# Performance work log

Hardware: AMD Instinct MI355X
Metric: run time of the kernel (lower is better)

The kernel has to match this reference:

```python
import jax, jax.numpy as jnp
import numpy as np

N_HEAD, D_MODEL, D_HEAD = 16, 1024, 64
BSZ, QLEN, KLEN = 4, 1024, 2048
MEM_LEN = KLEN - QLEN


def _rel_shift(x):
    # x: [b, q, k, n] -> Transformer-XL relative shift
    b, q, k, n = x.shape
    zero_pad = jnp.zeros((b, q, 1, n), dtype=x.dtype)
    x_padded = jnp.concatenate([zero_pad, x], axis=2)        # [b, q, k+1, n]
    x_padded = x_padded.reshape(b, k + 1, q, n)
    return x_padded[:, 1:].reshape(b, q, k, n)


def setup_inputs() -> dict:
    key = jax.random.key(0)
    ks = jax.random.split(key, 8)
    s = 0.02
    w = jax.random.normal(ks[0], (BSZ, KLEN, D_MODEL), jnp.float32)
    r = jax.random.normal(ks[1], (1, KLEN, D_MODEL), jnp.float32)
    r_w_bias = jax.random.normal(ks[2], (N_HEAD, D_HEAD), jnp.float32) * s
    r_r_bias = jax.random.normal(ks[3], (N_HEAD, D_HEAD), jnp.float32) * s
    Wq = jax.random.normal(ks[4], (D_MODEL, N_HEAD * D_HEAD), jnp.float32) * s
    Wkv = jax.random.normal(ks[5], (D_MODEL, 2 * N_HEAD * D_HEAD), jnp.float32) * s
    Wr = jax.random.normal(ks[6], (D_MODEL, N_HEAD * D_HEAD), jnp.float32) * s
    Wo = jax.random.normal(ks[7], (N_HEAD * D_HEAD, D_MODEL), jnp.float32) * s
    # causal mask with memory: query i attends to j <= i + MEM_LEN
    attn_mask = jnp.triu(jnp.ones((QLEN, KLEN), dtype=bool), k=MEM_LEN + 1)
    return {"w": w, "r": r, "r_w_bias": r_w_bias, "r_r_bias": r_r_bias,
            "Wq": Wq, "Wkv": Wkv, "Wr": Wr, "Wo": Wo,
            "attn_mask": attn_mask, "qlen": QLEN}


def reference(w, r, r_w_bias, r_r_bias, Wq, Wkv, Wr, Wo, attn_mask, qlen):
    bsz, klen, _ = w.shape
    rlen = r.shape[1]
    scale = 1.0 / (D_HEAD ** 0.5)

    q = (w[:, -qlen:] @ Wq).reshape(bsz, qlen, N_HEAD, D_HEAD)
    kv = w @ Wkv
    k, v = jnp.split(kv, 2, axis=-1)
    k = k.reshape(bsz, klen, N_HEAD, D_HEAD)
    v = v.reshape(bsz, klen, N_HEAD, D_HEAD)
    rk = (r[0] @ Wr).reshape(rlen, N_HEAD, D_HEAD)

    AC = jnp.einsum('bind,bjnd->bijn', q + r_w_bias, k)
    BD = jnp.einsum('bind,jnd->bijn', q + r_r_bias, rk)
    attn_score = (AC + _rel_shift(BD)) * scale
    attn_score = jnp.where(attn_mask[None, :, :, None], jnp.float32(-1e30), attn_score)
    attn_prob = jax.nn.softmax(attn_score, axis=2)
    attn_vec = jnp.einsum('bijn,bjnd->bind', attn_prob, v)
    attn_vec = attn_vec.reshape(bsz, qlen, N_HEAD * D_HEAD)
    return attn_vec @ Wo
```

## Files before the change

### kernel.cpp

```cpp
#include <hip/hip_runtime.h>

constexpr int BSZ  = 4;
constexpr int NH   = 16;
constexpr int DH   = 64;
constexpr int QL   = 1024;
constexpr int KLN  = 2048;
constexpr int DM   = 1024;
constexpr int MEM  = 1024;

typedef __bf16 bf16x8  __attribute__((ext_vector_type(8)));
typedef __bf16 bf16x4t __attribute__((ext_vector_type(4)));
typedef float  f32x4   __attribute__((ext_vector_type(4)));

__device__ __forceinline__ void g2l16(__bf16* lds, const __bf16* g) {
    __builtin_amdgcn_global_load_lds(
        (const __attribute__((address_space(1))) unsigned int*)g,
        (__attribute__((address_space(3))) unsigned int*)lds, 16, 0, 0);
}

__global__ __launch_bounds__(256)
void prep(const float* __restrict__ w, const float* __restrict__ r,
          const float* __restrict__ Wq, const float* __restrict__ Wr,
          const float* __restrict__ Wo, const float* __restrict__ Wkv,
          __bf16* __restrict__ wbh, __bf16* __restrict__ rbh,
          __bf16* __restrict__ WqT, __bf16* __restrict__ WrT,
          __bf16* __restrict__ WoT, __bf16* __restrict__ WkvT)
{
    __shared__ __bf16 t[64 * 72];
    const int id = blockIdx.x;
    if (id < 5120) {
        const float* in; __bf16* out; size_t i;
        if (id < 4096) { in = w; out = wbh; i = ((size_t)id * 256 + threadIdx.x) * 8; }
        else { in = r; out = rbh; i = ((size_t)(id - 4096) * 256 + threadIdx.x) * 8; }
        float4 a = *(const float4*)(in + i);
        float4 b = *(const float4*)(in + i + 4);
        bf16x8 y = {(__bf16)a.x, (__bf16)a.y, (__bf16)a.z, (__bf16)a.w,
                    (__bf16)b.x, (__bf16)b.y, (__bf16)b.z, (__bf16)b.w};
        *(bf16x8*)(out + i) = y;
        return;
    }
    const int tt = id - 5120;
    const int z = tt >> 9, rem = tt & 511;
    const int xx = rem & 31, yy = rem >> 5;
    const float* in; __bf16* out; int N;
    if (z == 0)      { in = Wq;  out = WqT;  N = 1024; }
    else if (z == 1) { in = Wr;  out = WrT;  N = 1024; }
    else if (z == 2) { in = Wo;  out = WoT;  N = 1024; }
    else             { in = Wkv; out = WkvT; N = 2048; }
    if (xx * 64 >= N) return;
    const int n0 = xx * 64, k0 = yy * 64;
    const int row = threadIdx.x >> 2, seg = (threadIdx.x & 3) << 4;
    const float* src = in + (long)(k0 + row) * N + n0 + seg;
#pragma unroll
    for (int u = 0; u < 16; u += 4) {
        float4 x = *(const float4*)(src + u);
        t[(seg + u + 0) * 72 + row] = (__bf16)x.x;
        t[(seg + u + 1) * 72 + row] = (__bf16)x.y;
        t[(seg + u + 2) * 72 + row] = (__bf16)x.z;
        t[(seg + u + 3) * 72 + row] = (__bf16)x.w;
    }
    __syncthreads();
    __bf16* dst = out + (long)(n0 + row) * 1024 + k0 + seg;
    *(uint4*)(dst)     = *(const uint4*)(t + row * 72 + seg);
    *(uint4*)(dst + 8) = *(const uint4*)(t + row * 72 + seg + 8);
}

__device__ __forceinline__ void gemm_core(
    const __bf16* __restrict__ A, const __bf16* __restrict__ BT,
    __bf16* As, __bf16* Bs, int m0, int n0, int K, f32x4 (&acc)[4][4])
{
    const int tid = threadIdx.x, w = tid >> 6, l = tid & 63;
    const int il = l & 15, quad = l >> 4;
    const int wm = (w >> 1) * 64, wn = (w & 1) * 64;
    const int lr = l >> 2, kc = (l & 3) ^ (lr & 3);

    const __bf16* ag = A  + (long)(m0 + w * 32 + lr) * K + kc * 8;
    const __bf16* bg = BT + (long)(n0 + w * 32 + lr) * K + kc * 8;
    __bf16* al0 = As + (w * 32) * 32;
    __bf16* al1 = As + (w * 32 + 16) * 32;
    __bf16* bl0 = Bs + (w * 32) * 32;
    __bf16* bl1 = Bs + (w * 32 + 16) * 32;
    const int rsw = il & 3;

    for (int k0 = 0; k0 < K; k0 += 32) {
        __syncthreads();
        g2l16(al0, ag + k0);
        g2l16(al1, ag + k0 + 16 * K);
        g2l16(bl0, bg + k0);
        g2l16(bl1, bg + k0 + 16 * K);
        __syncthreads();

        bf16x8 af[4], bf[4];
#pragma unroll
        for (int f = 0; f < 4; ++f) {
            af[f] = *(const bf16x8*)(As + (wm + f * 16 + il) * 32 + ((quad ^ rsw) << 3));
            bf[f] = *(const bf16x8*)(Bs + (wn + f * 16 + il) * 32 + ((quad ^ rsw) << 3));
        }
#pragma unroll
        for (int i = 0; i < 4; ++i)
#pragma unroll
            for (int j = 0; j < 4; ++j)
                acc[i][j] = __builtin_amdgcn_mfma_f32_16x16x32_bf16(
                    af[i], bf[j], acc[i][j], 0, 0, 0);
    }
}

__global__ __launch_bounds__(256, 2)
void gemm_proj(const __bf16* __restrict__ wbh, const __bf16* __restrict__ rbh,
               const __bf16* __restrict__ WqT, const __bf16* __restrict__ WkvT,
               const __bf16* __restrict__ WrT,
               __bf16* __restrict__ qwh, __bf16* __restrict__ qrh,
               __bf16* __restrict__ kh, __bf16* __restrict__ vhT,
               __bf16* __restrict__ rkh,
               const float* __restrict__ bw, const float* __restrict__ br)
{
    __shared__ __bf16 As[128 * 32];
    __shared__ __bf16 Bs[128 * 32];
    const int id = blockIdx.x;
    const __bf16 *A, *BT;
    int m0, n0, zz, kind;
    if (id < 1024) {
        n0 = (id & 15) * 128; m0 = ((id >> 4) & 15) * 128; zz = id >> 8;
        A = wbh + (size_t)zz * KLN * DM; BT = WkvT; kind = 3;
    } else if (id < 1280) {
        const int t = id - 1024;
        n0 = (t & 7) * 128; m0 = ((t >> 3) & 7) * 128; zz = t >> 6;
        A = wbh + (size_t)zz * KLN * DM + (size_t)MEM * DM; BT = WqT; kind = 2;
    } else {
        const int t = id - 1280;
        n0 = (t & 7) * 128; m0 = (t >> 3) * 128; zz = 0;
        A = rbh; BT = WrT; kind = 4;
    }

    f32x4 acc[4][4] = {};
    gemm_core(A, BT, As, Bs, m0, n0, DM, acc);

    const int tid = threadIdx.x, w = tid >> 6, l = tid & 63;
    const int il = l & 15, quad = l >> 4;
    const int wm = (w >> 1) * 64, wn = (w & 1) * 64;

    if (kind == 2) {
#pragma unroll
        for (int j = 0; j < 4; ++j) {
            const int col = n0 + wn + j * 16 + il;
            const int hn = col >> 6, d = col & 63;
            const float bwv = bw[col], brv = br[col];
            __bf16* q1 = qwh + ((size_t)(zz * 16 + hn) * 1024) * 64 + d;
            __bf16* q2 = qrh + ((size_t)(zz * 16 + hn) * 1024) * 64 + d;
#pragma unroll
            for (int i = 0; i < 4; ++i) {
                const int mb = m0 + wm + i * 16 + quad * 4;
#pragma unroll
                for (int rr = 0; rr < 4; ++rr) {
                    float v = acc[i][j][rr];
                    q1[(size_t)(mb + rr) * 64] = (__bf16)(v + bwv);
                    q2[(size_t)(mb + rr) * 64] = (__bf16)(v + brv);
                }
            }
        }
    } else if (kind == 3) {
        if (n0 + wn < 1024) {
#pragma unroll
            for (int j = 0; j < 4; ++j) {
                const int col = n0 + wn + j * 16 + il;
                const int hn = col >> 6, d = col & 63;
                __bf16* kp = kh + ((size_t)(zz * 16 + hn) * 2048) * 64 + d;
#pragma unroll
                for (int i = 0; i < 4; ++i) {
                    const int mb = m0 + wm + i * 16 + quad * 4;
#pragma unroll
                    for (int rr = 0; rr < 4; ++rr)
                        kp[(size_t)(mb + rr) * 64] = (__bf16)acc[i][j][rr];
                }
            }
        } else {
#pragma unroll
            for (int j = 0; j < 4; ++j) {
                const int col = n0 + wn + j * 16 + il - 1024;
                const int hn = col >> 6, d = col & 63;
                __bf16* vp = vhT + ((size_t)((zz * 16 + hn) * 64 + d)) * 2048;
#pragma unroll
                for (int i = 0; i < 4; ++i) {
                    const int mb = m0 + wm + i * 16 + quad * 4;
                    bf16x4t pk = {(__bf16)acc[i][j][0], (__bf16)acc[i][j][1],
                                  (__bf16)acc[i][j][2], (__bf16)acc[i][j][3]};
                    *(bf16x4t*)(vp + mb) = pk;
                }
            }
        }
    } else {
#pragma unroll
        for (int j = 0; j < 4; ++j) {
            const int col = n0 + wn + j * 16 + il;
            const int hn = col >> 6, d = col & 63;
            __bf16* rp = rkh + ((size_t)hn * 2048) * 64 + d;
#pragma unroll
            for (int i = 0; i < 4; ++i) {
                const int mb = m0 + wm + i * 16 + quad * 4;
#pragma unroll
                for (int rr = 0; rr < 4; ++rr)
                    rp[(size_t)(mb + rr) * 64] = (__bf16)acc[i][j][rr];
            }
        }
    }
}

__global__ __launch_bounds__(256, 2)
void gemm_out(const __bf16* __restrict__ avh, const __bf16* __restrict__ WoT,
              float* __restrict__ C)
{
    __shared__ __bf16 As[128 * 32];
    __shared__ __bf16 Bs[128 * 32];
    const int zz = blockIdx.z;
    const __bf16* A = avh + (size_t)zz * QL * DM;
    const int m0 = blockIdx.y * 128, n0 = blockIdx.x * 128;

    f32x4 acc[4][4] = {};
    gemm_core(A, WoT, As, Bs, m0, n0, DM, acc);

    const int tid = threadIdx.x, w = tid >> 6, l = tid & 63;
    const int il = l & 15, quad = l >> 4;
    const int wm = (w >> 1) * 64, wn = (w & 1) * 64;
    float* Cb = C + (size_t)zz * QL * DM;
#pragma unroll
    for (int i = 0; i < 4; ++i)
#pragma unroll
        for (int j = 0; j < 4; ++j) {
            float* cp = Cb + (long)(m0 + wm + i * 16 + quad * 4) * DM
                           + n0 + wn + j * 16 + il;
#pragma unroll
            for (int rr = 0; rr < 4; ++rr) cp[(long)rr * DM] = acc[i][j][rr];
        }
}

__global__ __launch_bounds__(256, 2)
void attn_mfma(const __bf16* __restrict__ qwh, const __bf16* __restrict__ qrh,
               const __bf16* __restrict__ kh, const __bf16* __restrict__ vhT,
               const __bf16* __restrict__ rkh, float* __restrict__ Op,
               float* __restrict__ ml)
{
    extern __shared__ __bf16 smem[];
    __bf16* kt  = smem;
    __bf16* vt  = smem + 4096;
    __bf16* rkt = smem + 8192;
    __bf16* sc  = smem + 20480;

    const int bx = blockIdx.x;
    const int part = bx & 1;
    const int bx2 = bx >> 1;
    const int ib = (bx2 & 1) ? (7 - (bx2 >> 1)) : (bx2 >> 1);
    const int i0 = ib * 128;
    const int n = blockIdx.y, b = blockIdx.z;
    const int tid = threadIdx.x;
    const int w = tid >> 6, l = tid & 63;
    const int il = l & 15, quad = l >> 4;
    const int iw0 = i0 + w * 32;

    bf16x8 qwf[2][2], qrf[2][2];
#pragma unroll
    for (int g = 0; g < 2; ++g) {
        const size_t qoff =
            ((size_t)((b * 16 + n) * QL + iw0 + 16 * g + il)) * 64 + quad * 8;
        qwf[g][0] = *(const bf16x8*)(qwh + qoff);
        qwf[g][1] = *(const bf16x8*)(qwh + qoff + 32);
        qrf[g][0] = *(const bf16x8*)(qrh + qoff);
        qrf[g][1] = *(const bf16x8*)(qrh + qoff + 32);
    }

    f32x4 O[2][4] = {};
    float m_i[2] = {-1e30f, -1e30f}, l_i[2] = {0.f, 0.f};
    const float c = 0.125f * 1.44269504f;

    const int srow = l >> 3, scl = l & 7;
    const __bf16* kbase  = kh  + ((size_t)((b * 16 + n) * KLN)) * 64;
    const __bf16* vbase0 = vhT + ((size_t)((b * 16 + n) * 64)) * KLN;
    const __bf16* rbp    = rkh + ((size_t)(n * KLN)) * 64;

    const int xk0 = ((quad) ^ (il & 7)) << 3;
    const int xk1 = ((quad + 4) ^ (il & 7)) << 3;

    const int nt = 2 * ib + 18;
    const int t0 = (part * nt) / 2;
    const int t1 = ((part + 1) * nt) / 2;
    int rot = (t0 % 3) * 64;

    const int ubB = 96 - 32 * w;

    for (int jt = t0; jt < t1; ++jt) {
        const int j0 = jt * 64;
        const int vu0 = j0 - i0 + 896;
        __syncthreads();
#pragma unroll
        for (int it = 0; it < 2; ++it) {
            const int row = w * 16 + it * 8 + srow;
            g2l16(kt + (w * 16 + it * 8) * 64,
                  kbase + ((size_t)(j0 + row)) * 64 + ((scl ^ srow) << 3));
        }
#pragma unroll
        for (int it = 0; it < 2; ++it) {
            const int row = w * 16 + it * 8 + srow;
            g2l16(vt + (w * 16 + it * 8) * 64,
                  vbase0 + (size_t)row * KLN + j0 + ((scl ^ srow) << 3));
        }
        if (jt == t0) {
#pragma unroll
            for (int it = 0; it < 6; ++it) {
                const int lbase = w * 48 + it * 8;
                int pb = lbase + rot; if (pb >= 192) pb -= 192;
                int vu = vu0 + lbase + srow;
                vu = vu < 0 ? 0 : (vu > KLN - 1 ? KLN - 1 : vu);
                g2l16(rkt + pb * 64,
                      rbp + (size_t)vu * 64 + ((scl ^ srow) << 3));
            }
        } else {
#pragma unroll
            for (int it = 0; it < 2; ++it) {
                const int lbase = 128 + w * 16 + it * 8;
                int pb = lbase + rot; if (pb >= 192) pb -= 192;
                int vu = vu0 + lbase + srow;
                vu = vu < 0 ? 0 : (vu > KLN - 1 ? KLN - 1 : vu);
                g2l16(rkt + pb * 64,
                      rbp + (size_t)vu * 64 + ((scl ^ srow) << 3));
            }
        }
        __syncthreads();

        const bool edge = (j0 + 63 > i0 + MEM);

        f32x4 sf[2][4];
#pragma unroll
        for (int fr = 0; fr < 4; ++fr) {
            const __bf16* ka = kt + (fr * 16 + il) * 64;
            bf16x8 a0 = *(const bf16x8*)(ka + xk0);
            bf16x8 a1 = *(const bf16x8*)(ka + xk1);
            __builtin_amdgcn_s_setprio(1);
#pragma unroll
            for (int g = 0; g < 2; ++g) {
                f32x4 acc = {};
                acc = __builtin_amdgcn_mfma_f32_16x16x32_bf16(a0, qwf[g][0], acc, 0, 0, 0);
                acc = __builtin_amdgcn_mfma_f32_16x16x32_bf16(a1, qwf[g][1], acc, 0, 0, 0);
                sf[g][fr] = acc;
            }
            __builtin_amdgcn_s_setprio(0);
        }

        {
            bf16x8 ra[6][2];
#pragma unroll
            for (int uf2 = 0; uf2 < 6; ++uf2) {
                int pr = ubB + uf2 * 16 + il + rot; if (pr >= 192) pr -= 192;
                const __bf16* rp_ = rkt + pr * 64;
                ra[uf2][0] = *(const bf16x8*)(rp_ + xk0);
                ra[uf2][1] = *(const bf16x8*)(rp_ + xk1);
            }
#pragma unroll
            for (int g = 0; g < 2; ++g) {
                __bf16* scg = sc + (w * 2 + g) * 1408;
#pragma unroll
                for (int uf = 0; uf < 5; ++uf) {
                    const int idx = uf + 1 - g;
                    f32x4 acc = {};
                    __builtin_amdgcn_s_setprio(1);
                    acc = __builtin_amdgcn_mfma_f32_16x16x32_bf16(ra[idx][0], qrf[g][0], acc, 0, 0, 0);
                    acc = __builtin_amdgcn_mfma_f32_16x16x32_bf16(ra[idx][1], qrf[g][1], acc, 0, 0, 0);
                    __builtin_amdgcn_s_setprio(0);
                    bf16x4t bb = {(__bf16)acc[0], (__bf16)acc[1],
                                  (__bf16)acc[2], (__bf16)acc[3]};
                    *(bf16x4t*)(scg + il * 88 + uf * 16 + quad * 4) = bb;
                }
            }
        }

        bf16x8 va[4][2];
#pragma unroll
        for (int df = 0; df < 4; ++df) {
            const __bf16* vp_ = vt + (df * 16 + il) * 64;
            va[df][0] = *(const bf16x8*)(vp_ + xk0);
            va[df][1] = *(const bf16x8*)(vp_ + xk1);
        }
#pragma unroll
        for (int g = 0; g < 2; ++g) {
            __bf16* scg = sc + (w * 2 + g) * 1408;
            const int i_gl = iw0 + 16 * g + il;

            float sv[4][4];
            float tmax = -1e30f;
#pragma unroll
            for (int fr = 0; fr < 4; ++fr)
#pragma unroll
                for (int rr = 0; rr < 4; ++rr) {
                    const int jl_ = fr * 16 + quad * 4 + rr;
                    float s = sf[g][fr][rr] + (float)scg[il * 88 + (jl_ - il + 15)];
                    if (edge) s = (j0 + jl_ > i_gl + MEM) ? -1e30f : s;
                    sv[fr][rr] = s;
                    tmax = fmaxf(tmax, s);
                }
            tmax = fmaxf(tmax, __shfl_xor(tmax, 16));
            tmax = fmaxf(tmax, __shfl_xor(tmax, 32));
            const float m_new = fmaxf(m_i[g], tmax);
            const float alpha = exp2f((m_i[g] - m_new) * c);
            float psum = 0.f;
#pragma unroll
            for (int fr = 0; fr < 4; ++fr) {
                bf16x4t p4;
#pragma unroll
                for (int rr = 0; rr < 4; ++rr) {
                    float p = exp2f((sv[fr][rr] - m_new) * c);
                    psum += p;
                    p4[rr] = (__bf16)p;
                }
                *(bf16x4t*)(scg + il * 88 + fr * 16 + quad * 4) = p4;
            }
            psum += __shfl_xor(psum, 16);
            psum += __shfl_xor(psum, 32);
            l_i[g] = l_i[g] * alpha + psum;
            m_i[g] = m_new;
#pragma unroll
            for (int df = 0; df < 4; ++df) O[g][df] *= alpha;

            bf16x8 p0 = *(const bf16x8*)(scg + il * 88 + quad * 8);
            bf16x8 p1 = *(const bf16x8*)(scg + il * 88 + 32 + quad * 8);
            __builtin_amdgcn_s_setprio(1);
#pragma unroll
            for (int df = 0; df < 4; ++df) {
                O[g][df] = __builtin_amdgcn_mfma_f32_16x16x32_bf16(va[df][0], p0, O[g][df], 0, 0, 0);
                O[g][df] = __builtin_amdgcn_mfma_f32_16x16x32_bf16(va[df][1], p1, O[g][df], 0, 0, 0);
            }
            __builtin_amdgcn_s_setprio(0);
        }
        rot += 64; if (rot >= 192) rot -= 192;
    }

#pragma unroll
    for (int g = 0; g < 2; ++g) {
        const int iL = w * 32 + 16 * g + il;
        float* opb = Op + (size_t)part * 4194304
                        + ((((size_t)b * NH + n) * 8 + ib)) * 8192
                        + (size_t)iL * 64 + quad * 4;
#pragma unroll
        for (int df = 0; df < 4; ++df)
            *(f32x4*)(opb + df * 16) = O[g][df];
        if (quad == 0) {
            const size_t base = (((size_t)b * NH + n) * 8 + ib) * 128 + iL;
            ml[(size_t)part * 65536 + base]          = m_i[g];
            ml[131072 + (size_t)part * 65536 + base] = l_i[g];
        }
    }
}

__global__ __launch_bounds__(256)
void attn_combine(const float* __restrict__ Op, const float* __restrict__ ml,
                  __bf16* __restrict__ av)
{
    const int tid = threadIdx.x;
    const int i = blockIdx.x * 4 + (tid >> 6);
    const int d = tid & 63;
    const int n = blockIdx.y, b = blockIdx.z;
    const int ib = i >> 7, iL = i & 127;
    const float c = 0.125f * 1.44269504f;

    const size_t mb = (((size_t)b * NH + n) * 8 + ib) * 128 + iL;
    const float m0 = ml[mb], m1 = ml[mb + 65536];
    const float l0 = ml[131072 + mb], l1 = ml[131072 + 65536 + mb];
    const float ms = fmaxf(m0, m1);
    const float w0 = exp2f((m0 - ms) * c);
    const float w1 = exp2f((m1 - ms) * c);
    const float ls = w0 * l0 + w1 * l1;

    const size_t ob = (((size_t)b * NH + n) * 8 + ib) * 8192
                      + (size_t)iL * 64 + d;
    const float o = w0 * Op[ob] + w1 * Op[ob + 4194304];
    av[((size_t)(b * QL + i)) * DM + n * 64 + d] = (__bf16)(o / ls);
}

extern "C" void kernel_launch(void* const* d_in, const int* in_sizes, int n_in,
                              void* d_out, int out_size, void* d_ws, size_t ws_size,
                              hipStream_t stream)
{
    const float* w   = (const float*)d_in[0];
    const float* r   = (const float*)d_in[1];
    const float* bwb = (const float*)d_in[2];
    const float* brb = (const float*)d_in[3];
    const float* Wq  = (const float*)d_in[4];
    const float* Wkv = (const float*)d_in[5];
    const float* Wr  = (const float*)d_in[6];
    const float* Wo  = (const float*)d_in[7];
    float* out = (float*)d_out;

    char* ws = (char*)d_ws;
    __bf16* wbh  = (__bf16*)(ws);
    __bf16* rbh  = (__bf16*)(ws + ((size_t)16 << 20));
    __bf16* WqT  = (__bf16*)(ws + ((size_t)20 << 20));
    __bf16* WkvT = (__bf16*)(ws + ((size_t)22 << 20));
    __bf16* WrT  = (__bf16*)(ws + ((size_t)26 << 20));
    __bf16* WoT  = (__bf16*)(ws + ((size_t)28 << 20));
    __bf16* qwh  = (__bf16*)(ws + ((size_t)30 << 20));
    __bf16* qrh  = (__bf16*)(ws + ((size_t)38 << 20));
    __bf16* kh   = (__bf16*)(ws + ((size_t)46 << 20));
    __bf16* vhT  = (__bf16*)(ws + ((size_t)62 << 20));
    __bf16* rkh  = (__bf16*)(ws + ((size_t)78 << 20));
    __bf16* avh  = (__bf16*)(ws + ((size_t)82 << 20));
    float*  Op   = (float*)(ws + ((size_t)90 << 20));
    float*  mlb  = (float*)(ws + ((size_t)122 << 20));

    dim3 blk(256);
    prep<<<7168, blk, 0, stream>>>(w, r, Wq, Wr, Wo, Wkv,
                                   wbh, rbh, WqT, WrT, WoT, WkvT);
    gemm_proj<<<1408, blk, 0, stream>>>(wbh, rbh, WqT, WkvT, WrT,
                                        qwh, qrh, kh, vhT, rkh, bwb, brb);
    attn_mfma<<<dim3(16, 16, 4), blk, 63488, stream>>>(
        qwh, qrh, kh, vhT, rkh, Op, mlb);
    attn_combine<<<dim3(256, 16, 4), blk, 0, stream>>>(Op, mlb, avh);
    gemm_out<<<dim3(8, 8, 4), blk, 0, stream>>>(avh, WoT, out);
}
```

Baseline: 375.6 us.

## Double-buffer K/V tiles and prefetch the next tile in the attention loop

The attention kernel now keeps two K/V LDS buffers and widens the relative-key ring from 192 to 256 rows, so ring indexing becomes a bitmask. It issues the async global-to-LDS loads for the next tile before computing on the current one, which cuts the loop to a single barrier per iteration. The aim is to hide global load latency behind MFMA and softmax work. The per-wave score scratch is also shared across the two row groups, and the positional MFMA is moved next to its use. The cost is more LDS per block (76.8 KB), which could limit residency to two blocks per CU, and correctness now depends on the async loads completing before the next barrier.

```diff
diff --git a/kernel.cpp b/kernel.cpp
--- a/kernel.cpp
+++ b/kernel.cpp
@@ -241,9 +241,9 @@
 {
     extern __shared__ __bf16 smem[];
     __bf16* kt  = smem;
-    __bf16* vt  = smem + 4096;
-    __bf16* rkt = smem + 8192;
-    __bf16* sc  = smem + 20480;
+    __bf16* vt  = smem + 8192;
+    __bf16* rkt = smem + 16384;
+    __bf16* sc  = smem + 32768;
 
     const int bx = blockIdx.x;
     const int part = bx & 1;
@@ -282,14 +282,13 @@
     const int nt = 2 * ib + 18;
     const int t0 = (part * nt) / 2;
     const int t1 = ((part + 1) * nt) / 2;
-    int rot = (t0 % 3) * 64;
+    int rot = 0;
 
     const int ubB = 96 - 32 * w;
 
-    for (int jt = t0; jt < t1; ++jt) {
-        const int j0 = jt * 64;
+    {
+        const int j0 = t0 * 64;
         const int vu0 = j0 - i0 + 896;
-        __syncthreads();
 #pragma unroll
         for (int it = 0; it < 2; ++it) {
             const int row = w * 16 + it * 8 + srow;
@@ -302,35 +301,56 @@
             g2l16(vt + (w * 16 + it * 8) * 64,
                   vbase0 + (size_t)row * KLN + j0 + ((scl ^ srow) << 3));
         }
-        if (jt == t0) {
-#pragma unroll
-            for (int it = 0; it < 6; ++it) {
-                const int lbase = w * 48 + it * 8;
-                int pb = lbase + rot; if (pb >= 192) pb -= 192;
-                int vu = vu0 + lbase + srow;
+#pragma unroll
+        for (int it = 0; it < 6; ++it) {
+            const int lbase = w * 48 + it * 8;
+            int vu = vu0 + lbase + srow;
+            vu = vu < 0 ? 0 : (vu > KLN - 1 ? KLN - 1 : vu);
+            g2l16(rkt + lbase * 64,
+                  rbp + (size_t)vu * 64 + ((scl ^ srow) << 3));
+        }
+    }
+
+    int cur = 0;
+    for (int jt = t0; jt < t1; ++jt) {
+        const int j0 = jt * 64;
+        __syncthreads();
+
+        if (jt + 1 < t1) {
+            const int j0n = j0 + 64;
+            const int nxt = cur ^ 1;
+#pragma unroll
+            for (int it = 0; it < 2; ++it) {
+                const int row = w * 16 + it * 8 + srow;
+                g2l16(kt + nxt * 4096 + (w * 16 + it * 8) * 64,
+                      kbase + ((size_t)(j0n + row)) * 64 + ((scl ^ srow) << 3));
+            }
+#pragma unroll
+            for (int it = 0; it < 2; ++it) {
+                const int row = w * 16 + it * 8 + srow;
+                g2l16(vt + nxt * 4096 + (w * 16 + it * 8) * 64,
+                      vbase0 + (size_t)row * KLN + j0n + ((scl ^ srow) << 3));
+            }
+            const int vu0n = j0n - i0 + 896;
+#pragma unroll
+            for (int it = 0; it < 2; ++it) {
+                const int lbase = 128 + w * 16 + it * 8;
+                const int pb = (rot + 64 + lbase) & 255;
+                int vu = vu0n + lbase + srow;
                 vu = vu < 0 ? 0 : (vu > KLN - 1 ? KLN - 1 : vu);
                 g2l16(rkt + pb * 64,
                       rbp + (size_t)vu * 64 + ((scl ^ srow) << 3));
             }
-        } else {
-#pragma unroll
-            for (int it = 0; it < 2; ++it) {
-                const int lbase = 128 + w * 16 + it * 8;
-                int pb = lbase + rot; if (pb >= 192) pb -= 192;
-                int vu = vu0 + lbase + srow;
-                vu = vu < 0 ? 0 : (vu > KLN - 1 ? KLN - 1 : vu);
-                g2l16(rkt + pb * 64,
-                      rbp + (size_t)vu * 64 + ((scl ^ srow) << 3));
-            }
-        }
-        __syncthreads();
-
+        }
+
+        const __bf16* ktc = kt + cur * 4096;
+        const __bf16* vtc = vt + cur * 4096;
         const bool edge = (j0 + 63 > i0 + MEM);
 
         f32x4 sf[2][4];
 #pragma unroll
         for (int fr = 0; fr < 4; ++fr) {
-            const __bf16* ka = kt + (fr * 16 + il) * 64;
+            const __bf16* ka = ktc + (fr * 16 + il) * 64;
             bf16x8 a0 = *(const bf16x8*)(ka + xk0);
             bf16x8 a1 = *(const bf16x8*)(ka + xk1);
             __builtin_amdgcn_s_setprio(1);
@@ -344,45 +364,39 @@
             __builtin_amdgcn_s_setprio(0);
         }
 
-        {
-            bf16x8 ra[6][2];
-#pragma unroll
-            for (int uf2 = 0; uf2 < 6; ++uf2) {
-                int pr = ubB + uf2 * 16 + il + rot; if (pr >= 192) pr -= 192;
-                const __bf16* rp_ = rkt + pr * 64;
-                ra[uf2][0] = *(const bf16x8*)(rp_ + xk0);
-                ra[uf2][1] = *(const bf16x8*)(rp_ + xk1);
-            }
-#pragma unroll
-            for (int g = 0; g < 2; ++g) {
-                __bf16* scg = sc + (w * 2 + g) * 1408;
-#pragma unroll
-                for (int uf = 0; uf < 5; ++uf) {
-                    const int idx = uf + 1 - g;
-                    f32x4 acc = {};
-                    __builtin_amdgcn_s_setprio(1);
-                    acc = __builtin_amdgcn_mfma_f32_16x16x32_bf16(ra[idx][0], qrf[g][0], acc, 0, 0, 0);
-                    acc = __builtin_amdgcn_mfma_f32_16x16x32_bf16(ra[idx][1], qrf[g][1], acc, 0, 0, 0);
-                    __builtin_amdgcn_s_setprio(0);
-                    bf16x4t bb = {(__bf16)acc[0], (__bf16)acc[1],
-                                  (__bf16)acc[2], (__bf16)acc[3]};
-                    *(bf16x4t*)(scg + il * 88 + uf * 16 + quad * 4) = bb;
-                }
-            }
-        }
-
+        bf16x8 ra[6][2];
+#pragma unroll
+        for (int uf2 = 0; uf2 < 6; ++uf2) {
+            const int pr = (ubB + uf2 * 16 + il + rot) & 255;
+            const __bf16* rp_ = rkt + pr * 64;
+            ra[uf2][0] = *(const bf16x8*)(rp_ + xk0);
+            ra[uf2][1] = *(const bf16x8*)(rp_ + xk1);
+        }
         bf16x8 va[4][2];
 #pragma unroll
         for (int df = 0; df < 4; ++df) {
-            const __bf16* vp_ = vt + (df * 16 + il) * 64;
+            const __bf16* vp_ = vtc + (df * 16 + il) * 64;
             va[df][0] = *(const bf16x8*)(vp_ + xk0);
             va[df][1] = *(const bf16x8*)(vp_ + xk1);
         }
+
+        __bf16* scw = sc + w * 1408;
 #pragma unroll
         for (int g = 0; g < 2; ++g) {
-            __bf16* scg = sc + (w * 2 + g) * 1408;
+#pragma unroll
+            for (int uf = 0; uf < 5; ++uf) {
+                const int idx = uf + 1 - g;
+                f32x4 acc = {};
+                __builtin_amdgcn_s_setprio(1);
+                acc = __builtin_amdgcn_mfma_f32_16x16x32_bf16(ra[idx][0], qrf[g][0], acc, 0, 0, 0);
+                acc = __builtin_amdgcn_mfma_f32_16x16x32_bf16(ra[idx][1], qrf[g][1], acc, 0, 0, 0);
+                __builtin_amdgcn_s_setprio(0);
+                bf16x4t bb = {(__bf16)acc[0], (__bf16)acc[1],
+                              (__bf16)acc[2], (__bf16)acc[3]};
+                *(bf16x4t*)(scw + il * 88 + uf * 16 + quad * 4) = bb;
+            }
+
             const int i_gl = iw0 + 16 * g + il;
-
             float sv[4][4];
             float tmax = -1e30f;
 #pragma unroll
@@ -390,7 +404,7 @@
 #pragma unroll
                 for (int rr = 0; rr < 4; ++rr) {
                     const int jl_ = fr * 16 + quad * 4 + rr;
-                    float s = sf[g][fr][rr] + (float)scg[il * 88 + (jl_ - il + 15)];
+                    float s = sf[g][fr][rr] + (float)scw[il * 88 + (jl_ - il + 15)];
                     if (edge) s = (j0 + jl_ > i_gl + MEM) ? -1e30f : s;
                     sv[fr][rr] = s;
                     tmax = fmaxf(tmax, s);
@@ -409,7 +423,7 @@
                     psum += p;
                     p4[rr] = (__bf16)p;
                 }
-                *(bf16x4t*)(scg + il * 88 + fr * 16 + quad * 4) = p4;
+                *(bf16x4t*)(scw + il * 88 + fr * 16 + quad * 4) = p4;
             }
             psum += __shfl_xor(psum, 16);
             psum += __shfl_xor(psum, 32);
@@ -418,8 +432,8 @@
 #pragma unroll
             for (int df = 0; df < 4; ++df) O[g][df] *= alpha;
 
-            bf16x8 p0 = *(const bf16x8*)(scg + il * 88 + quad * 8);
-            bf16x8 p1 = *(const bf16x8*)(scg + il * 88 + 32 + quad * 8);
+            bf16x8 p0 = *(const bf16x8*)(scw + il * 88 + quad * 8);
+            bf16x8 p1 = *(const bf16x8*)(scw + il * 88 + 32 + quad * 8);
             __builtin_amdgcn_s_setprio(1);
 #pragma unroll
             for (int df = 0; df < 4; ++df) {
@@ -428,7 +442,8 @@
             }
             __builtin_amdgcn_s_setprio(0);
         }
-        rot += 64; if (rot >= 192) rot -= 192;
+        rot = (rot + 64) & 255;
+        cur ^= 1;
     }
 
 #pragma unroll
@@ -508,7 +523,7 @@
                                    wbh, rbh, WqT, WrT, WoT, WkvT);
     gemm_proj<<<1408, blk, 0, stream>>>(wbh, rbh, WqT, WkvT, WrT,
                                         qwh, qrh, kh, vhT, rkh, bwb, brb);
-    attn_mfma<<<dim3(16, 16, 4), blk, 63488, stream>>>(
+    attn_mfma<<<dim3(16, 16, 4), blk, 76800, stream>>>(
         qwh, qrh, kh, vhT, rkh, Op, mlb);
     attn_combine<<<dim3(256, 16, 4), blk, 0, stream>>>(Op, mlb, avh);
     gemm_out<<<dim3(8, 8, 4), blk, 0, stream>>>(avh, WoT, out);
```

Result: no change. 377.8 us (+0.6%).
